# Kernel optimization log

Measured on AMD Instinct MI355X. Metric: run time of the kernel, lower is better.

The kernel has to match this reference:

```python
import jax, jax.numpy as jnp
import numpy as np

NH = 8       # num_heads
KS = 7       # kernel_size (odd)
DIM = 256


def setup_inputs() -> dict:
    key = jax.random.key(0)
    ks = jax.random.split(key, 8)
    B, H, W, C = 2, 56, 56, DIM
    x_q = jax.random.normal(ks[0], (B, H, W, C), jnp.float32)
    x_k = jax.random.normal(ks[1], (B, H, W, C), jnp.float32)
    # small-scale weights so softmax logits stay in a sane range
    Wq = jax.random.normal(ks[2], (C, C), jnp.float32) * 0.02
    bq = jnp.zeros((C,), jnp.float32)
    Wkv = jax.random.normal(ks[3], (C, 2 * C), jnp.float32) * 0.02
    bkv = jnp.zeros((2 * C,), jnp.float32)
    rpb = jax.random.normal(ks[4], (NH, 2 * KS - 1, 2 * KS - 1), jnp.float32) * 0.02
    Wproj = jax.random.normal(ks[5], (C, C), jnp.float32) * 0.02
    bproj = jnp.zeros((C,), jnp.float32)
    return {"x_q": x_q, "x_k": x_k, "Wq": Wq, "bq": bq, "Wkv": Wkv,
            "bkv": bkv, "rpb": rpb, "Wproj": Wproj, "bproj": bproj}


def _neighborhood_idx(n, k):
    # NATTEN clamped window (dilation=1): start_i = clip(i - k//2, 0, n - k)
    start = jnp.clip(jnp.arange(n) - k // 2, 0, n - k)          # [n]
    idx = start[:, None] + jnp.arange(k)[None, :]               # [n, k] key positions
    bidx = idx - jnp.arange(n)[:, None] + (k - 1)               # [n, k] rpb index (rel offset + k-1)
    return idx, bidx


def reference(x_q, x_k, Wq, bq, Wkv, bkv, rpb, Wproj, bproj):
    B, H, W, C = x_q.shape
    hd = C // NH
    scale = hd ** -0.5
    # projections
    q = (x_q @ Wq + bq).reshape(B, H, W, NH, hd).transpose(0, 3, 1, 2, 4) * scale  # [B,nh,H,W,hd]
    kv = (x_k @ Wkv + bkv).reshape(B, H, W, 2, NH, hd)
    kk = kv[..., 0, :, :].transpose(0, 3, 1, 2, 4)   # [B,nh,H,W,hd]
    vv = kv[..., 1, :, :].transpose(0, 3, 1, 2, 4)   # [B,nh,H,W,hd]

    idx_h, bi = _neighborhood_idx(H, KS)   # [H,KS]
    idx_w, bj = _neighborhood_idx(W, KS)   # [W,KS]

    # gather neighborhoods: [B,nh,H,W,KS,KS,hd]
    Kn = kk[:, :, idx_h[:, None, :, None], idx_w[None, :, None, :], :]
    Vn = vv[:, :, idx_h[:, None, :, None], idx_w[None, :, None, :], :]
    # relative position bias: [nh,H,W,KS,KS]
    bias = rpb[:, bi[:, None, :, None], bj[None, :, None, :]]

    attn = jnp.einsum('bnijd,bnijkld->bnijkl', q, Kn) + bias[None]
    attn = jax.nn.softmax(attn.reshape(B, NH, H, W, KS * KS), axis=-1)
    attn = attn.reshape(B, NH, H, W, KS, KS)
    out = jnp.einsum('bnijkl,bnijkld->bnijd', attn, Vn)     # [B,nh,H,W,hd]
    out = out.transpose(0, 2, 3, 1, 4).reshape(B, H, W, C)
    return out @ Wproj + bproj
```

## Files before the change

kernel.cpp:

```cpp
#include <hip/hip_runtime.h>
#include <hip/hip_bf16.h>

#define NHEAD 8
#define KSZ 7
#define HS 56
#define WS 56
#define MTOK (2 * HS * WS)

typedef unsigned short u16;
typedef unsigned int u32;

using bf16x8 = __attribute__((ext_vector_type(8))) short;
using f32x4  = __attribute__((ext_vector_type(4))) float;

static __device__ __forceinline__ u16 f2bf(float x) {
    u32 u = __float_as_uint(x);
    u += 0x7FFFu + ((u >> 16) & 1u);
    return (u16)(u >> 16);
}
static __device__ __forceinline__ float bf2f(u16 h) {
    return __uint_as_float(((u32)h) << 16);
}

static __device__ __forceinline__ void gload16(const void* g, void* l) {
    __builtin_amdgcn_global_load_lds(
        (const __attribute__((address_space(1))) u32*)g,
        (__attribute__((address_space(3))) u32*)l, 16, 0, 0);
}

__global__ __launch_bounds__(256) void cvt_w_kernel(
    const float* __restrict__ Wq, const float* __restrict__ Wkv,
    const float* __restrict__ Wp,
    u16* __restrict__ WT, u16* __restrict__ WpT_h, u16* __restrict__ WpT_l)
{
    __shared__ float Ts[32][33];
    const int b = blockIdx.x;
    const float* W; u16 *Th, *Tl; int N, tile; bool wantlo;
    if (b < 64)       { W = Wq;  Th = WT;             Tl = nullptr; N = 256; tile = b;       wantlo = false; }
    else if (b < 192) { W = Wkv; Th = WT + 256 * 256; Tl = nullptr; N = 512; tile = b - 64;  wantlo = false; }
    else              { W = Wp;  Th = WpT_h;          Tl = WpT_l;   N = 256; tile = b - 192; wantlo = true; }
    const int ntiles_n = N / 32;
    const int k0 = (tile / ntiles_n) * 32;
    const int n0 = (tile % ntiles_n) * 32;

    const int t = threadIdx.x;
    {
        const int kk = t >> 3, nn4 = (t & 7) * 4;
        float4 v = *reinterpret_cast<const float4*>(&W[(size_t)(k0 + kk) * N + n0 + nn4]);
        Ts[kk][nn4 + 0] = v.x; Ts[kk][nn4 + 1] = v.y;
        Ts[kk][nn4 + 2] = v.z; Ts[kk][nn4 + 3] = v.w;
    }
    __syncthreads();
    {
        const int nn = t >> 3, kk4 = (t & 7) * 4;
        const int n = n0 + nn;
        ushort4 h, l;
        u16* hp = &h.x; u16* lp = &l.x;
        #pragma unroll
        for (int i = 0; i < 4; ++i) {
            float x = Ts[kk4 + i][nn];
            u16 hb = f2bf(x);
            hp[i] = hb;
            lp[i] = f2bf(x - bf2f(hb));
        }
        const int kg = k0 + kk4;
        const int kphys = (kg & ~63) | ((((kg >> 3) & 7) ^ (n & 7)) << 3) | (kg & 7);
        const size_t o = (size_t)n * 256 + kphys;
        *reinterpret_cast<ushort4*>(&Th[o]) = h;
        if (wantlo) *reinterpret_cast<ushort4*>(&Tl[o]) = l;
    }
}

__global__ __launch_bounds__(256) void gemm_qkv_kernel(
    const float* __restrict__ Aq, const float* __restrict__ Akv,
    const u16* __restrict__ WT,
    const float* __restrict__ biasq, const float* __restrict__ biaskv,
    float* __restrict__ outq, float* __restrict__ outkv, float scale)
{
    __shared__ __align__(16) u16 AS[64 * 64];
    __shared__ __align__(16) u16 BS[128 * 64];

    const int tid  = threadIdx.x;
    const int lane = tid & 63;
    const int w    = tid >> 6;
    const int l16  = lane & 15;
    const int lhi  = lane >> 4;

    const int n0 = blockIdx.x * 128;
    const int m0 = blockIdx.y * 64;

    const float* A32 = (n0 < 256) ? Aq : Akv;

    const int arow = tid >> 2;
    const int akc  = (tid & 3) * 16;
    const int ac0  = (tid & 3) * 2;
    const int aswz = arow & 7;

    f32x4 acc[4][2];
    #pragma unroll
    for (int mi = 0; mi < 4; ++mi)
        #pragma unroll
        for (int ni = 0; ni < 2; ++ni) acc[mi][ni] = (f32x4){0.f, 0.f, 0.f, 0.f};

    for (int kt = 0; kt < 256; kt += 64) {
        __syncthreads();

        #pragma unroll
        for (int i = 0; i < 4; ++i) {
            const int rbase = w * 32 + i * 8;
            const size_t src = (size_t)(n0 + rbase + (lane >> 3)) * 256 + kt + (lane & 7) * 8;
            gload16(WT + src, &BS[rbase * 64]);
        }

        {
            const float* ap = &A32[(size_t)(m0 + arow) * 256 + kt + akc];
            float f[16];
            #pragma unroll
            for (int v = 0; v < 4; ++v) {
                float4 t = *reinterpret_cast<const float4*>(ap + v * 4);
                f[v * 4 + 0] = t.x; f[v * 4 + 1] = t.y;
                f[v * 4 + 2] = t.z; f[v * 4 + 3] = t.w;
            }
            union { u16 u[8]; uint4 v; } hx[2];
            #pragma unroll
            for (int e = 0; e < 16; ++e) hx[e >> 3].u[e & 7] = f2bf(f[e]);
            #pragma unroll
            for (int c = 0; c < 2; ++c) {
                const int o = arow * 64 + (((ac0 + c) ^ aswz) << 3);
                *reinterpret_cast<uint4*>(&AS[o]) = hx[c].v;
            }
        }

        __syncthreads();

        #pragma unroll
        for (int ks = 0; ks < 2; ++ks) {
            const int cph = ((ks * 4 + lhi) ^ (l16 & 7)) << 3;
            bf16x8 ah[4], bh[2];
            #pragma unroll
            for (int mi = 0; mi < 4; ++mi)
                ah[mi] = *reinterpret_cast<const bf16x8*>(&AS[(mi * 16 + l16) * 64 + cph]);
            #pragma unroll
            for (int ni = 0; ni < 2; ++ni)
                bh[ni] = *reinterpret_cast<const bf16x8*>(&BS[(w * 32 + ni * 16 + l16) * 64 + cph]);
            #pragma unroll
            for (int mi = 0; mi < 4; ++mi)
                #pragma unroll
                for (int ni = 0; ni < 2; ++ni)
                    acc[mi][ni] = __builtin_amdgcn_mfma_f32_16x16x32_bf16(
                        ah[mi], bh[ni], acc[mi][ni], 0, 0, 0);
        }
    }

    const bool isq = (n0 < 256);
    float* op = isq ? outq : outkv;
    const float* bs = isq ? biasq : biaskv;
    const int ldo = isq ? 256 : 512;
    const int coff = isq ? 0 : 256;
    const float sc = isq ? scale : 1.0f;

    #pragma unroll
    for (int ni = 0; ni < 2; ++ni) {
        const int col = n0 + w * 32 + ni * 16 + l16 - coff;
        const float bv = bs[col];
        #pragma unroll
        for (int mi = 0; mi < 4; ++mi) {
            const int row = m0 + mi * 16 + lhi * 4;
            #pragma unroll
            for (int rg = 0; rg < 4; ++rg)
                op[(size_t)(row + rg) * ldo + col] = (acc[mi][ni][rg] + bv) * sc;
        }
    }
}

__global__ __launch_bounds__(256) void gemm_proj_kernel(
    const u16* __restrict__ Ah, const u16* __restrict__ Al,
    const u16* __restrict__ Wh, const u16* __restrict__ Wl,
    const float* __restrict__ bias, float* __restrict__ out)
{
    __shared__ __align__(16) u16 AhS[64 * 64];
    __shared__ __align__(16) u16 AlS[64 * 64];
    __shared__ __align__(16) u16 BhS[128 * 64];
    __shared__ __align__(16) u16 BlS[128 * 64];

    const int tid  = threadIdx.x;
    const int lane = tid & 63;
    const int w    = tid >> 6;
    const int l16  = lane & 15;
    const int lhi  = lane >> 4;

    const int n0 = blockIdx.x * 128;
    const int m0 = blockIdx.y * 64;

    f32x4 acc[4][2];
    #pragma unroll
    for (int mi = 0; mi < 4; ++mi)
        #pragma unroll
        for (int ni = 0; ni < 2; ++ni) acc[mi][ni] = (f32x4){0.f, 0.f, 0.f, 0.f};

    for (int kt = 0; kt < 256; kt += 64) {
        __syncthreads();

        #pragma unroll
        for (int i = 0; i < 4; ++i) {
            const int rbase = w * 32 + i * 8;
            const size_t src = (size_t)(n0 + rbase + (lane >> 3)) * 256 + kt + (lane & 7) * 8;
            gload16(Wh + src, &BhS[rbase * 64]);
            gload16(Wl + src, &BlS[rbase * 64]);
        }
        #pragma unroll
        for (int i = 0; i < 2; ++i) {
            const int rbase = w * 16 + i * 8;
            const size_t src = (size_t)(m0 + rbase + (lane >> 3)) * 256 + kt + (lane & 7) * 8;
            gload16(Ah + src, &AhS[rbase * 64]);
            gload16(Al + src, &AlS[rbase * 64]);
        }

        __syncthreads();

        #pragma unroll
        for (int ks = 0; ks < 2; ++ks) {
            const int cph = ((ks * 4 + lhi) ^ (l16 & 7)) << 3;
            bf16x8 ah[4], al[4], bh[2], bl[2];
            #pragma unroll
            for (int mi = 0; mi < 4; ++mi) {
                const int ro = (mi * 16 + l16) * 64 + cph;
                ah[mi] = *reinterpret_cast<const bf16x8*>(&AhS[ro]);
                al[mi] = *reinterpret_cast<const bf16x8*>(&AlS[ro]);
            }
            #pragma unroll
            for (int ni = 0; ni < 2; ++ni) {
                const int ro = (w * 32 + ni * 16 + l16) * 64 + cph;
                bh[ni] = *reinterpret_cast<const bf16x8*>(&BhS[ro]);
                bl[ni] = *reinterpret_cast<const bf16x8*>(&BlS[ro]);
            }
            #pragma unroll
            for (int mi = 0; mi < 4; ++mi)
                #pragma unroll
                for (int ni = 0; ni < 2; ++ni) {
                    acc[mi][ni] = __builtin_amdgcn_mfma_f32_16x16x32_bf16(
                        ah[mi], bh[ni], acc[mi][ni], 0, 0, 0);
                    acc[mi][ni] = __builtin_amdgcn_mfma_f32_16x16x32_bf16(
                        ah[mi], bl[ni], acc[mi][ni], 0, 0, 0);
                    acc[mi][ni] = __builtin_amdgcn_mfma_f32_16x16x32_bf16(
                        al[mi], bh[ni], acc[mi][ni], 0, 0, 0);
                }
        }
    }

    #pragma unroll
    for (int ni = 0; ni < 2; ++ni) {
        const int col = n0 + w * 32 + ni * 16 + l16;
        const float bv = bias[col];
        #pragma unroll
        for (int mi = 0; mi < 4; ++mi) {
            const int row = m0 + mi * 16 + lhi * 4;
            #pragma unroll
            for (int rg = 0; rg < 4; ++rg)
                out[(size_t)(row + rg) * 256 + col] = acc[mi][ni][rg] + bv;
        }
    }
}

#define REG 14
#define NREG (REG*REG)
#define KST 36

__global__ __launch_bounds__(256) void natten_kernel(
    const float* __restrict__ qb, const float* __restrict__ kvb,
    const float* __restrict__ rpb,
    u16* __restrict__ ohi, u16* __restrict__ olo)
{
    __shared__ float Ks[NREG * KST];
    __shared__ float Rp[169];

    const int tid = threadIdx.x;
    const int bid = blockIdx.x;
    const int head = bid & 7;
    const int idx  = bid >> 3;
    const int b    = idx / 49;
    const int t49  = idx % 49;
    const int ti0  = (t49 / 7) * 8;
    const int tj0  = (t49 % 7) * 8;

    int gr0 = ti0 - 3; gr0 = gr0 < 0 ? 0 : gr0; gr0 = gr0 > HS - REG ? HS - REG : gr0;
    int gc0 = tj0 - 3; gc0 = gc0 < 0 ? 0 : gc0; gc0 = gc0 > WS - REG ? WS - REG : gc0;

    const float* kvb_head = kvb + (size_t)b * 3136 * 512 + head * 32;

    #pragma unroll
    for (int rt0 = 0; rt0 < NREG; rt0 += 32) {
        const int rt = rt0 + (tid >> 3);
        if (rt < NREG) {
            const int r = rt / REG, c = rt % REG;
            const int g = (gr0 + r) * WS + (gc0 + c);
            const float4 v = *reinterpret_cast<const float4*>(
                kvb_head + (size_t)g * 512 + (tid & 7) * 4);
            *reinterpret_cast<float4*>(&Ks[rt * KST + (tid & 7) * 4]) = v;
        }
    }
    if (tid < 169) Rp[tid] = rpb[head * 169 + tid];

    const int tokl = tid >> 2;
    const int q4   = tid & 3;
    const int tr = tokl >> 3, tc = tokl & 7;
    const int i = ti0 + tr, j = tj0 + tc;

    int si = i - 3; si = si < 0 ? 0 : si; si = si > HS - KSZ ? HS - KSZ : si;
    int sj = j - 3; sj = sj < 0 ? 0 : sj; sj = sj > WS - KSZ ? WS - KSZ : sj;

    const int nb0 = (si - gr0) * REG + (sj - gc0);
    const int rb0 = (si - i + 6) * 13 + (sj - j + 6);
    const int tokflat = b * 3136 + i * WS + j;

    const float* qp = qb + (size_t)tokflat * 256 + head * 32 + q4 * 8;
    const float4 qv0 = *reinterpret_cast<const float4*>(qp);
    const float4 qv1 = *reinterpret_cast<const float4*>(qp + 4);

    __syncthreads();

    float lg[49];
    #pragma unroll
    for (int ki = 0; ki < KSZ; ++ki) {
        #pragma unroll
        for (int kj = 0; kj < KSZ; ++kj) {
            const float* kp = &Ks[(nb0 + ki * REG + kj) * KST + q4 * 8];
            const float4 k0 = *reinterpret_cast<const float4*>(kp);
            const float4 k1 = *reinterpret_cast<const float4*>(kp + 4);
            float p = qv0.x * k0.x;
            p = fmaf(qv0.y, k0.y, p);
            p = fmaf(qv0.z, k0.z, p);
            p = fmaf(qv0.w, k0.w, p);
            p = fmaf(qv1.x, k1.x, p);
            p = fmaf(qv1.y, k1.y, p);
            p = fmaf(qv1.z, k1.z, p);
            p = fmaf(qv1.w, k1.w, p);
            p += __shfl_xor(p, 1);
            p += __shfl_xor(p, 2);
            lg[ki * 7 + kj] = p + Rp[rb0 + ki * 13 + kj];
        }
    }

    float m = -1e30f;
    #pragma unroll
    for (int l = 0; l < 49; ++l) m = fmaxf(m, lg[l]);
    float ssum = 0.f;
    #pragma unroll
    for (int l = 0; l < 49; ++l) {
        const float e = __expf(lg[l] - m);
        lg[l] = e;
        ssum += e;
    }

    __syncthreads();

    #pragma unroll
    for (int rt0 = 0; rt0 < NREG; rt0 += 32) {
        const int rt = rt0 + (tid >> 3);
        if (rt < NREG) {
            const int r = rt / REG, c = rt % REG;
            const int g = (gr0 + r) * WS + (gc0 + c);
            const float4 v = *reinterpret_cast<const float4*>(
                kvb_head + (size_t)g * 512 + 256 + (tid & 7) * 4);
            *reinterpret_cast<float4*>(&Ks[rt * KST + (tid & 7) * 4]) = v;
        }
    }
    __syncthreads();

    float acc[8] = {0.f, 0.f, 0.f, 0.f, 0.f, 0.f, 0.f, 0.f};
    #pragma unroll
    for (int ki = 0; ki < KSZ; ++ki) {
        #pragma unroll
        for (int kj = 0; kj < KSZ; ++kj) {
            const float w = lg[ki * 7 + kj];
            const float* vp = &Ks[(nb0 + ki * REG + kj) * KST + q4 * 8];
            const float4 v0 = *reinterpret_cast<const float4*>(vp);
            const float4 v1 = *reinterpret_cast<const float4*>(vp + 4);
            acc[0] = fmaf(w, v0.x, acc[0]);
            acc[1] = fmaf(w, v0.y, acc[1]);
            acc[2] = fmaf(w, v0.z, acc[2]);
            acc[3] = fmaf(w, v0.w, acc[3]);
            acc[4] = fmaf(w, v1.x, acc[4]);
            acc[5] = fmaf(w, v1.y, acc[5]);
            acc[6] = fmaf(w, v1.z, acc[6]);
            acc[7] = fmaf(w, v1.w, acc[7]);
        }
    }

    const float inv = 1.f / ssum;
    union { u16 u[8]; uint4 v; } ph, pl;
    #pragma unroll
    for (int d = 0; d < 8; ++d) {
        const float x = acc[d] * inv;
        const u16 hb = f2bf(x);
        ph.u[d] = hb;
        pl.u[d] = f2bf(x - bf2f(hb));
    }
    const int chunk = head * 4 + q4;
    const int seg = chunk >> 3, cin = chunk & 7;
    const int cphys = cin ^ (tokflat & 7);
    const size_t o = (size_t)tokflat * 256 + seg * 64 + cphys * 8;
    *reinterpret_cast<uint4*>(&ohi[o]) = ph.v;
    *reinterpret_cast<uint4*>(&olo[o]) = pl.v;
}

extern "C" void kernel_launch(void* const* d_in, const int* in_sizes, int n_in,
                              void* d_out, int out_size, void* d_ws, size_t ws_size,
                              hipStream_t stream) {
    const float* x_q   = (const float*)d_in[0];
    const float* x_k   = (const float*)d_in[1];
    const float* Wq    = (const float*)d_in[2];
    const float* bq    = (const float*)d_in[3];
    const float* Wkv   = (const float*)d_in[4];
    const float* bkv   = (const float*)d_in[5];
    const float* rpb   = (const float*)d_in[6];
    const float* Wproj = (const float*)d_in[7];
    const float* bproj = (const float*)d_in[8];
    float* out = (float*)d_out;

    const int M = MTOK;

    float* qbuf  = (float*)d_ws;
    float* kvbuf = qbuf + (size_t)M * 256;
    u16* at_hi   = (u16*)(kvbuf + (size_t)M * 512);
    u16* at_lo   = at_hi + (size_t)M * 256;
    u16* WT      = at_lo + (size_t)M * 256;
    u16* WpT_h   = WT + 768 * 256;
    u16* WpT_l   = WpT_h + 256 * 256;

    const float scale = 0.17677669529663687f;

    dim3 blk(256);
    cvt_w_kernel<<<dim3(256), blk, 0, stream>>>(Wq, Wkv, Wproj, WT, WpT_h, WpT_l);

    gemm_qkv_kernel<<<dim3(6, M / 64), blk, 0, stream>>>(
        x_q, x_k, WT, bq, bkv, qbuf, kvbuf, scale);

    natten_kernel<<<dim3(784), blk, 0, stream>>>(qbuf, kvbuf, rpb, at_hi, at_lo);

    gemm_proj_kernel<<<dim3(2, M / 64), blk, 0, stream>>>(
        at_hi, at_lo, WpT_h, WpT_l, bproj, out);
}
```

Before: 54.03 us.

## Add XCD-aware block swizzle, prefetch A tiles, shrink proj GEMM tiles

```diff
diff --git a/kernel.cpp b/kernel.cpp
--- a/kernel.cpp
+++ b/kernel.cpp
@@ -26,6 +26,12 @@
     __builtin_amdgcn_global_load_lds(
         (const __attribute__((address_space(1))) u32*)g,
         (__attribute__((address_space(3))) u32*)l, 16, 0, 0);
+}
+
+static __device__ __forceinline__ int xcd_swz(int bid, int nwg) {
+    const int q = nwg >> 3, r = nwg & 7;
+    const int x = bid & 7, o = bid >> 3;
+    return (x < r ? x * (q + 1) : r * (q + 1) + (x - r) * q) + o;
 }
 
 __global__ __launch_bounds__(256) void cvt_w_kernel(
@@ -86,8 +92,9 @@
     const int l16  = lane & 15;
     const int lhi  = lane >> 4;
 
-    const int n0 = blockIdx.x * 128;
-    const int m0 = blockIdx.y * 64;
+    const int swz = xcd_swz(blockIdx.x, 6 * (MTOK / 64));
+    const int n0 = (swz % 6) * 128;
+    const int m0 = (swz / 6) * 64;
 
     const float* A32 = (n0 < 256) ? Aq : Akv;
 
@@ -95,6 +102,7 @@
     const int akc  = (tid & 3) * 16;
     const int ac0  = (tid & 3) * 2;
     const int aswz = arow & 7;
+    const float* aptr = &A32[(size_t)(m0 + arow) * 256 + akc];
 
     f32x4 acc[4][2];
     #pragma unroll
@@ -102,6 +110,12 @@
         #pragma unroll
         for (int ni = 0; ni < 2; ++ni) acc[mi][ni] = (f32x4){0.f, 0.f, 0.f, 0.f};
 
+    float4 fa[4];
+    #pragma unroll
+    for (int v = 0; v < 4; ++v)
+        fa[v] = *reinterpret_cast<const float4*>(aptr + v * 4);
+
+    #pragma unroll
     for (int kt = 0; kt < 256; kt += 64) {
         __syncthreads();
 
@@ -112,15 +126,18 @@
             gload16(WT + src, &BS[rbase * 64]);
         }
 
+        float4 fn[4];
+        if (kt < 192) {
+            #pragma unroll
+            for (int v = 0; v < 4; ++v)
+                fn[v] = *reinterpret_cast<const float4*>(aptr + kt + 64 + v * 4);
+        }
+
         {
-            const float* ap = &A32[(size_t)(m0 + arow) * 256 + kt + akc];
-            float f[16];
-            #pragma unroll
-            for (int v = 0; v < 4; ++v) {
-                float4 t = *reinterpret_cast<const float4*>(ap + v * 4);
-                f[v * 4 + 0] = t.x; f[v * 4 + 1] = t.y;
-                f[v * 4 + 2] = t.z; f[v * 4 + 3] = t.w;
-            }
+            const float f[16] = {fa[0].x, fa[0].y, fa[0].z, fa[0].w,
+                                 fa[1].x, fa[1].y, fa[1].z, fa[1].w,
+                                 fa[2].x, fa[2].y, fa[2].z, fa[2].w,
+                                 fa[3].x, fa[3].y, fa[3].z, fa[3].w};
             union { u16 u[8]; uint4 v; } hx[2];
             #pragma unroll
             for (int e = 0; e < 16; ++e) hx[e >> 3].u[e & 7] = f2bf(f[e]);
@@ -150,6 +167,9 @@
                     acc[mi][ni] = __builtin_amdgcn_mfma_f32_16x16x32_bf16(
                         ah[mi], bh[ni], acc[mi][ni], 0, 0, 0);
         }
+
+        #pragma unroll
+        for (int v = 0; v < 4; ++v) fa[v] = fn[v];
     }
 
     const bool isq = (n0 < 256);
@@ -180,40 +200,40 @@
 {
     __shared__ __align__(16) u16 AhS[64 * 64];
     __shared__ __align__(16) u16 AlS[64 * 64];
-    __shared__ __align__(16) u16 BhS[128 * 64];
-    __shared__ __align__(16) u16 BlS[128 * 64];
+    __shared__ __align__(16) u16 BhS[64 * 64];
+    __shared__ __align__(16) u16 BlS[64 * 64];
 
     const int tid  = threadIdx.x;
     const int lane = tid & 63;
     const int w    = tid >> 6;
+    const int wm   = w >> 1;
+    const int wn   = w & 1;
     const int l16  = lane & 15;
     const int lhi  = lane >> 4;
 
-    const int n0 = blockIdx.x * 128;
-    const int m0 = blockIdx.y * 64;
-
-    f32x4 acc[4][2];
-    #pragma unroll
-    for (int mi = 0; mi < 4; ++mi)
+    const int swz = xcd_swz(blockIdx.x, 4 * (MTOK / 64));
+    const int n0 = (swz % 4) * 64;
+    const int m0 = (swz / 4) * 64;
+
+    f32x4 acc[2][2];
+    #pragma unroll
+    for (int mi = 0; mi < 2; ++mi)
         #pragma unroll
         for (int ni = 0; ni < 2; ++ni) acc[mi][ni] = (f32x4){0.f, 0.f, 0.f, 0.f};
 
+    #pragma unroll
     for (int kt = 0; kt < 256; kt += 64) {
         __syncthreads();
 
         #pragma unroll
-        for (int i = 0; i < 4; ++i) {
-            const int rbase = w * 32 + i * 8;
-            const size_t src = (size_t)(n0 + rbase + (lane >> 3)) * 256 + kt + (lane & 7) * 8;
-            gload16(Wh + src, &BhS[rbase * 64]);
-            gload16(Wl + src, &BlS[rbase * 64]);
-        }
-        #pragma unroll
         for (int i = 0; i < 2; ++i) {
             const int rbase = w * 16 + i * 8;
-            const size_t src = (size_t)(m0 + rbase + (lane >> 3)) * 256 + kt + (lane & 7) * 8;
-            gload16(Ah + src, &AhS[rbase * 64]);
-            gload16(Al + src, &AlS[rbase * 64]);
+            const size_t srcB = (size_t)(n0 + rbase + (lane >> 3)) * 256 + kt + (lane & 7) * 8;
+            const size_t srcA = (size_t)(m0 + rbase + (lane >> 3)) * 256 + kt + (lane & 7) * 8;
+            gload16(Wh + srcB, &BhS[rbase * 64]);
+            gload16(Wl + srcB, &BlS[rbase * 64]);
+            gload16(Ah + srcA, &AhS[rbase * 64]);
+            gload16(Al + srcA, &AlS[rbase * 64]);
         }
 
         __syncthreads();
@@ -221,21 +241,21 @@
         #pragma unroll
         for (int ks = 0; ks < 2; ++ks) {
             const int cph = ((ks * 4 + lhi) ^ (l16 & 7)) << 3;
-            bf16x8 ah[4], al[4], bh[2], bl[2];
-            #pragma unroll
-            for (int mi = 0; mi < 4; ++mi) {
-                const int ro = (mi * 16 + l16) * 64 + cph;
+            bf16x8 ah[2], al[2], bh[2], bl[2];
+            #pragma unroll
+            for (int mi = 0; mi < 2; ++mi) {
+                const int ro = (wm * 32 + mi * 16 + l16) * 64 + cph;
                 ah[mi] = *reinterpret_cast<const bf16x8*>(&AhS[ro]);
                 al[mi] = *reinterpret_cast<const bf16x8*>(&AlS[ro]);
             }
             #pragma unroll
             for (int ni = 0; ni < 2; ++ni) {
-                const int ro = (w * 32 + ni * 16 + l16) * 64 + cph;
+                const int ro = (wn * 32 + ni * 16 + l16) * 64 + cph;
                 bh[ni] = *reinterpret_cast<const bf16x8*>(&BhS[ro]);
                 bl[ni] = *reinterpret_cast<const bf16x8*>(&BlS[ro]);
             }
             #pragma unroll
-            for (int mi = 0; mi < 4; ++mi)
+            for (int mi = 0; mi < 2; ++mi)
                 #pragma unroll
                 for (int ni = 0; ni < 2; ++ni) {
                     acc[mi][ni] = __builtin_amdgcn_mfma_f32_16x16x32_bf16(
@@ -250,11 +270,11 @@
 
     #pragma unroll
     for (int ni = 0; ni < 2; ++ni) {
-        const int col = n0 + w * 32 + ni * 16 + l16;
+        const int col = n0 + wn * 32 + ni * 16 + l16;
         const float bv = bias[col];
         #pragma unroll
-        for (int mi = 0; mi < 4; ++mi) {
-            const int row = m0 + mi * 16 + lhi * 4;
+        for (int mi = 0; mi < 2; ++mi) {
+            const int row = m0 + wm * 32 + mi * 16 + lhi * 4;
             #pragma unroll
             for (int rg = 0; rg < 4; ++rg)
                 out[(size_t)(row + rg) * 256 + col] = acc[mi][ni][rg] + bv;
@@ -433,11 +453,11 @@
     dim3 blk(256);
     cvt_w_kernel<<<dim3(256), blk, 0, stream>>>(Wq, Wkv, Wproj, WT, WpT_h, WpT_l);
 
-    gemm_qkv_kernel<<<dim3(6, M / 64), blk, 0, stream>>>(
+    gemm_qkv_kernel<<<dim3(6 * (M / 64)), blk, 0, stream>>>(
         x_q, x_k, WT, bq, bkv, qbuf, kvbuf, scale);
 
     natten_kernel<<<dim3(784), blk, 0, stream>>>(qbuf, kvbuf, rpb, at_hi, at_lo);
 
-    gemm_proj_kernel<<<dim3(2, M / 64), blk, 0, stream>>>(
+    gemm_proj_kernel<<<dim3(4 * (M / 64)), blk, 0, stream>>>(
         at_hi, at_lo, WpT_h, WpT_l, bproj, out);
 }
```

After: 51.40 us. 4.9% less time.
